# Optimization experiments

Measured on AMD Instinct MI355X. Metric: run time of the kernel, lower is better.

Reference implementation:

```python
import jax, jax.numpy as jnp
import numpy as np

C = 96        # dim
HEADS = 8     # FrameHistoryRouter heads (StateAlignBlock forces heads=1)
WS = 4        # window_size = 2*scale_patchsize
NFC = 1       # num_frames_tocache
TOPK = 5
LOCAL_N = 4


def conv(x, w, stride=1, pad=0, groups=1):
    return jax.lax.conv_general_dilated(
        x, w, (stride, stride), [(pad, pad), (pad, pad)],
        dimension_numbers=("NCHW", "OIHW", "NCHW"), feature_group_count=groups)


def l2norm(x, axis):
    n = jnp.linalg.norm(x, axis=axis, keepdims=True)
    return x / jnp.maximum(n, 1e-12)


def setup_inputs() -> dict:
    key = jax.random.key(0)
    ks = jax.random.split(key, 16)
    def rn(i, shp, s=0.02):
        return jax.random.normal(ks[i], shp, dtype=jnp.float32) * s
    return {
        "x": jax.random.normal(ks[0], (2, C, 256, 256), dtype=jnp.float32),
        "sab_qk_w": rn(1, (2 * C, C, 1, 1)),
        "sab_qk_dw": rn(2, (2 * C, 1, 3, 3)),
        "sab_v_w": rn(3, (C, C, 1, 1)),
        "sab_v_dw": rn(4, (C, 1, 3, 3)),
        "sab_k2_w": rn(5, (2 * C, C, 1, 1)),
        "sab_k2_dw": rn(6, (2 * C, 1, WS, WS)),
        "sab_q2_w": rn(7, (2 * C, C, 1, 1)),
        "sab_q2_dw": rn(8, (2 * C, 1, WS, WS)),
        "sab_proj_w": rn(9, (C, C, 1, 1)),
        "sab_temp": jnp.ones((1, 1, 1), jnp.float32),
        "fhr_qkv_w": rn(10, (3 * C, C, 1, 1)),
        "fhr_qkv_dw": rn(11, (3 * C, 1, 3, 3)),
        "fhr_proj_w": rn(12, (C, C, 1, 1)),
        "fhr_temp": jnp.ones((HEADS, 1, 1), jnp.float32),
    }


def _forward(x, sab_qk_w, sab_qk_dw, sab_v_w, sab_v_dw, sab_k2_w, sab_k2_dw,
             sab_q2_w, sab_q2_dw, sab_proj_w, sab_temp,
             fhr_qkv_w, fhr_qkv_dw, fhr_proj_w, fhr_temp):
    b, c, h, w = x.shape
    # ---------- StateAlignBlock (no cache: first frame) ----------
    qk = conv(conv(x, sab_qk_w), sab_qk_dw, pad=1, groups=2 * c)
    q, k = jnp.split(qk, 2, axis=1)
    v = conv(conv(x, sab_v_w), sab_v_dw, pad=1, groups=c)
    k = conv(conv(k, sab_k2_w), sab_k2_dw, stride=WS, pad=1, groups=2 * c)
    q = conv(conv(q, sab_q2_w), sab_q2_dw, stride=WS, pad=1, groups=2 * c)
    H, W = q.shape[2], q.shape[3]            # = h//WS, w//WS
    N = H * W
    # b (1 d) h w -> b 1 1 (h w) d   with d = 2c
    q = q.reshape(b, 2 * c, N).transpose(0, 2, 1)[:, None, None]
    k = k.reshape(b, 2 * c, N).transpose(0, 2, 1)[:, None, None]
    # v: b (1 d) (p1 h) (p2 w) -> b 1 1 (h w) (p1 p2 d), p1=p2=WS, d=c
    h2, w2 = h // WS, w // WS
    v = v.reshape(b, c, WS, h2, WS, w2).transpose(0, 3, 5, 2, 4, 1)
    v = v.reshape(b, 1, 1, h2 * w2, WS * WS * c)
    q = l2norm(q, -1)
    k = l2norm(k, -1)
    attn = jnp.einsum("bfgnd,bfgmd->bfgnm", q, k) * sab_temp  # [b,1,1,N,N]
    # zero_out_non_top_k (top-5 along last dim; threshold form, ties negligible)
    kth = jax.lax.top_k(attn, TOPK)[0][..., TOPK - 1:TOPK]
    topk_mask = (attn >= kth).astype(attn.dtype)
    # local attention mask: manhattan distance <= LOCAL_N on the HxW patch grid
    yy, xx = jnp.meshgrid(jnp.arange(H), jnp.arange(W), indexing="ij")
    coords = jnp.stack([yy.ravel(), xx.ravel()], axis=-1)          # [N,2]
    dist = jnp.abs(coords[:, None, :] - coords[None, :, :]).sum(-1)
    local = (dist <= LOCAL_N).astype(attn.dtype)                   # [N,N]
    attn = attn * topk_mask + attn * local                         # as in torch
    # clipped_softmax
    zero = attn == 0
    s = jax.nn.softmax(jnp.where(zero, -jnp.inf, attn), axis=-1)
    s = jnp.where(zero, 0.0, s)
    s = s / s.sum(-1, keepdims=True)
    out = jnp.einsum("bfgnm,bfgmd->bfgnd", s, v)  # [b,1,1,N, WS*WS*c]
    F = 1  # curr_num_frames (no cache)
    # b f 1 (h w) (p1 p2 d) -> (b f) d (p1 h) (p2 w)
    out = out.reshape(b * F, h2, w2, WS, WS, c).transpose(0, 5, 3, 1, 4, 2)
    out = out.reshape(b * F, c, h, w)
    out = conv(out, sab_proj_w)
    aligned = out.reshape(b, F, c, h, w)
    k_s = k[:, -NFC:]  # [b,1,1,N,2c]
    v_s = v[:, -NFC:]
    # ---------- FrameHistoryRouter on aligned current frame ----------
    x2 = aligned[:, -1]
    qkv = conv(conv(x2, fhr_qkv_w), fhr_qkv_dw, pad=1, groups=3 * c)
    q2, k2, v2 = jnp.split(qkv, 3, axis=1)
    hd = c // HEADS
    q2 = q2.reshape(b, HEADS, hd, h * w)
    k2 = k2.reshape(b, HEADS, hd, h * w)
    v2 = v2.reshape(b, HEADS, hd, h * w)
    q2 = l2norm(q2, -1)
    k2 = l2norm(k2, -1)
    a2 = jnp.einsum("bhcn,bhdn->bhcd", q2, k2) * fhr_temp  # [b,H,hd,hd]
    a2 = jax.nn.softmax(a2, axis=-1)
    o2 = jnp.einsum("bhcd,bhdn->bhcn", a2, v2).reshape(b, c, h, w)
    o2 = conv(o2, fhr_proj_w)
    keep = int(NFC * c / HEADS)  # = hd
    return o2, k_s, v_s, k2[:, :, -keep:, :], v2[:, :, -keep:, :]


def reference(x, sab_qk_w, sab_qk_dw, sab_v_w, sab_v_dw, sab_k2_w, sab_k2_dw,
              sab_q2_w, sab_q2_dw, sab_proj_w, sab_temp,
              fhr_qkv_w, fhr_qkv_dw, fhr_proj_w, fhr_temp):
    return _forward(x, sab_qk_w, sab_qk_dw, sab_v_w, sab_v_dw, sab_k2_w,
                    sab_k2_dw, sab_q2_w, sab_q2_dw, sab_proj_w, sab_temp,
                    fhr_qkv_w, fhr_qkv_dw, fhr_proj_w, fhr_temp)
```

## Files before the change

kernel.cpp:

```cpp
#include <hip/hip_runtime.h>
#include <hip/hip_bf16.h>
#include <math.h>

#define HW 65536L

typedef __attribute__((ext_vector_type(8))) short bf16x8;
typedef __attribute__((ext_vector_type(4))) float f32x4;

__device__ __forceinline__ int iabs_(int v) { return v < 0 ? -v : v; }

__global__ __launch_bounds__(256) void wsplit(
    const float* __restrict__ qk, const float* __restrict__ v,
    const float* __restrict__ q2, const float* __restrict__ k2,
    const float* __restrict__ pj, const float* __restrict__ fq,
    const float* __restrict__ fp, unsigned short* __restrict__ whl)
{
  const int e = blockIdx.x*256 + threadIdx.x;
  if (e >= 110592) return;
  const int row = e / 96, col = e - row*96;
  float f;
  if      (row <  192) f = qk[e];
  else if (row <  288) f = v [(row-192)*96+col];
  else if (row <  480) f = q2[(row-288)*96+col];
  else if (row <  672) f = k2[(row-480)*96+col];
  else if (row <  768) f = pj[(row-672)*96+col];
  else if (row < 1056) f = fq[(row-768)*96+col];
  else                 f = fp[(row-1056)*96+col];
  __hip_bfloat16 h = __float2bfloat16(f);
  float hf = __bfloat162float(h);
  __hip_bfloat16 l = __float2bfloat16(f - hf);
  whl[e]          = *(unsigned short*)&h;
  whl[110592 + e] = *(unsigned short*)&l;
}

#define BLDS 104
__global__ __launch_bounds__(256) void conv1x1_mfma(
    const float* __restrict__ in, long in_bstride,
    const unsigned short* __restrict__ whl, int wrow0,
    float* __restrict__ out, long out_bstride,
    float* __restrict__ out2, long out2_bstride, int msplit,
    int mtiles, int mode)
{
  __shared__ unsigned short bhs[128*BLDS];
  __shared__ unsigned short bls[128*BLDS];
  const int t = threadIdx.x;
  const int p0 = blockIdx.x * 128;
  const int b = blockIdx.y;
  if (mode == 0) {
    #pragma unroll
    for (int it = 0; it < 6; it++) {
      const int idx = it*256 + t;
      const int g8 = idx >> 7;
      const int pix = idx & 127;
      const float* src = in + (long)b*in_bstride + (long)(g8*8)*HW + p0 + pix;
      unsigned hh[8], ll[8];
      #pragma unroll
      for (int j = 0; j < 8; j++) {
        float f = src[(long)j*HW];
        unsigned u = __float_as_uint(f);
        hh[j] = u >> 16;
        float lof = f - __uint_as_float(u & 0xFFFF0000u);
        __hip_bfloat16 lb = __float2bfloat16(lof);
        ll[j] = *(unsigned short*)&lb;
      }
      uint4 hv, lv;
      hv.x = hh[0]|(hh[1]<<16); hv.y = hh[2]|(hh[3]<<16);
      hv.z = hh[4]|(hh[5]<<16); hv.w = hh[6]|(hh[7]<<16);
      lv.x = ll[0]|(ll[1]<<16); lv.y = ll[2]|(ll[3]<<16);
      lv.z = ll[4]|(ll[5]<<16); lv.w = ll[6]|(ll[7]<<16);
      *(uint4*)(bhs + pix*BLDS + g8*8) = hv;
      *(uint4*)(bls + pix*BLDS + g8*8) = lv;
    }
  } else {
    const int pp = t >> 1, half = (t & 1)*48;
    const int p = p0 + pp;
    const int py = p >> 8, px = p & 255;
    const float* src = in + (long)b*in_bstride
        + ((long)((py & 63)*64 + (px & 63))*16 + ((py >> 6)*4 + (px >> 6)))*96 + half;
    #pragma unroll
    for (int j4 = 0; j4 < 12; j4++) {
      float4 v4 = *(const float4*)&src[j4*4];
      float fv[4] = {v4.x, v4.y, v4.z, v4.w};
      unsigned hh[4], ll[4];
      #pragma unroll
      for (int u4 = 0; u4 < 4; u4++) {
        unsigned u = __float_as_uint(fv[u4]);
        hh[u4] = u >> 16;
        float lof = fv[u4] - __uint_as_float(u & 0xFFFF0000u);
        __hip_bfloat16 lb = __float2bfloat16(lof);
        ll[u4] = *(unsigned short*)&lb;
      }
      uint2 hv, lv;
      hv.x = hh[0] | (hh[1] << 16); hv.y = hh[2] | (hh[3] << 16);
      lv.x = ll[0] | (ll[1] << 16); lv.y = ll[2] | (ll[3] << 16);
      *(uint2*)(bhs + pp*BLDS + half + j4*4) = hv;
      *(uint2*)(bls + pp*BLDS + half + j4*4) = lv;
    }
  }
  __syncthreads();
  const int lane = t & 63, w = t >> 6;
  const int fr = lane & 15, fk = lane >> 4;
  bf16x8 Bh[2][3], Bl[2][3];
  #pragma unroll
  for (int nt = 0; nt < 2; nt++)
    #pragma unroll
    for (int kt = 0; kt < 3; kt++) {
      const int pix = w*32 + nt*16 + fr;
      Bh[nt][kt] = *(const bf16x8*)(bhs + pix*BLDS + kt*32 + fk*8);
      Bl[nt][kt] = *(const bf16x8*)(bls + pix*BLDS + kt*32 + fk*8);
    }
  for (int m = 0; m < mtiles; m++) {
    const long wbase = (long)(wrow0 + m*16 + fr)*96 + fk*8;
    bf16x8 Ah[3], Al[3];
    #pragma unroll
    for (int kt = 0; kt < 3; kt++) {
      Ah[kt] = *(const bf16x8*)(whl + wbase + kt*32);
      Al[kt] = *(const bf16x8*)(whl + 110592 + wbase + kt*32);
    }
    f32x4 acc[2] = {};
    #pragma unroll
    for (int nt = 0; nt < 2; nt++)
      #pragma unroll
      for (int kt = 0; kt < 3; kt++) {
        acc[nt] = __builtin_amdgcn_mfma_f32_16x16x32_bf16(Ah[kt], Bh[nt][kt], acc[nt], 0, 0, 0);
        acc[nt] = __builtin_amdgcn_mfma_f32_16x16x32_bf16(Ah[kt], Bl[nt][kt], acc[nt], 0, 0, 0);
        acc[nt] = __builtin_amdgcn_mfma_f32_16x16x32_bf16(Al[kt], Bh[nt][kt], acc[nt], 0, 0, 0);
      }
    const int mo = (m < msplit) ? m : (m - msplit);
    float* dst = ((m < msplit) ? out + (long)b*out_bstride
                               : out2 + (long)b*out2_bstride) + p0 + w*32;
    #pragma unroll
    for (int nt = 0; nt < 2; nt++)
      #pragma unroll
      for (int r = 0; r < 4; r++)
        dst[(long)(mo*16 + fk*4 + r)*HW + nt*16 + fr] = acc[nt][r];
  }
}

__global__ __launch_bounds__(256) void dw3x3v(
    const float* __restrict__ in, int inCH, const float* __restrict__ w,
    float* __restrict__ out, int outCH)
{
  const int t = threadIdx.x;
  const int p4 = blockIdx.x * 256 + t;
  const int ch = blockIdx.y, b = blockIdx.z;
  const int y = p4 >> 6, x0 = (p4 & 63) << 2;
  const float* ip = in + ((long)b*inCH + ch) * HW;
  const float* wp = w + ch*9;
  float a0 = 0.f, a1 = 0.f, a2 = 0.f, a3 = 0.f;
  #pragma unroll
  for (int dy = -1; dy <= 1; dy++) {
    const int yy = y + dy;
    if (yy < 0 || yy > 255) continue;
    const float* rp = ip + yy*256;
    const float4 c = *(const float4*)&rp[x0];
    const float left  = (x0 > 0)   ? rp[x0-1] : 0.f;
    const float right = (x0 < 252) ? rp[x0+4] : 0.f;
    const float w0 = wp[(dy+1)*3+0], w1 = wp[(dy+1)*3+1], w2 = wp[(dy+1)*3+2];
    a0 = fmaf(left, w0, a0); a0 = fmaf(c.x, w1, a0); a0 = fmaf(c.y, w2, a0);
    a1 = fmaf(c.x,  w0, a1); a1 = fmaf(c.y, w1, a1); a1 = fmaf(c.z, w2, a1);
    a2 = fmaf(c.y,  w0, a2); a2 = fmaf(c.z, w1, a2); a2 = fmaf(c.w, w2, a2);
    a3 = fmaf(c.z,  w0, a3); a3 = fmaf(c.w, w1, a3); a3 = fmaf(right, w2, a3);
  }
  float4 o; o.x = a0; o.y = a1; o.z = a2; o.w = a3;
  *(float4*)&out[((long)b*outCH + ch)*HW + y*256 + x0] = o;
}

__global__ __launch_bounds__(256) void dw3x3_vs(
    const float* __restrict__ in, const float* __restrict__ w,
    float* __restrict__ vs)
{
  __shared__ float tile[96*65];
  const int t = threadIdx.x;
  const int gb = blockIdx.x;
  const int b = blockIdx.y;
  const int y = gb >> 2, xb = gb & 3;
  #pragma unroll
  for (int i = 0; i < 6; i++) {
    const int idx = i*256 + t;
    const int ci = idx >> 4, q = idx & 15;
    const int x0 = xb*64 + q*4;
    const float* ip = in + ((long)b*96 + ci) * HW;
    const float* wp = w + ci*9;
    float a0 = 0.f, a1 = 0.f, a2 = 0.f, a3 = 0.f;
    #pragma unroll
    for (int dy = -1; dy <= 1; dy++) {
      const int yy = y + dy;
      if (yy < 0 || yy > 255) continue;
      const float* rp = ip + yy*256;
      const float4 c = *(const float4*)&rp[x0];
      const float left  = (x0 > 0)   ? rp[x0-1] : 0.f;
      const float right = (x0 < 252) ? rp[x0+4] : 0.f;
      const float w0 = wp[(dy+1)*3+0], w1 = wp[(dy+1)*3+1], w2 = wp[(dy+1)*3+2];
      a0 = fmaf(left, w0, a0); a0 = fmaf(c.x, w1, a0); a0 = fmaf(c.y, w2, a0);
      a1 = fmaf(c.x,  w0, a1); a1 = fmaf(c.y, w1, a1); a1 = fmaf(c.z, w2, a1);
      a2 = fmaf(c.y,  w0, a2); a2 = fmaf(c.z, w1, a2); a2 = fmaf(c.w, w2, a2);
      a3 = fmaf(c.z,  w0, a3); a3 = fmaf(c.w, w1, a3); a3 = fmaf(right, w2, a3);
    }
    const int xl = q*4;
    tile[ci*65 + xl    ] = a0;
    tile[ci*65 + xl + 1] = a1;
    tile[ci*65 + xl + 2] = a2;
    tile[ci*65 + xl + 3] = a3;
  }
  __syncthreads();
  const int blk = (y >> 6)*4 + xb;
  float* obase = vs + ((long)b*4096 + (long)(y & 63)*64) * 1536 + blk*96;
  #pragma unroll
  for (int i = 0; i < 24; i++) {
    const int idx = i*256 + t;
    const int nl = idx / 96, ci = idx % 96;
    obase[(long)nl*1536 + ci] = tile[ci*65 + nl];
  }
}

__global__ __launch_bounds__(256) void dw4x4s4v(
    const float* __restrict__ in, const float* __restrict__ w,
    float* __restrict__ out)
{
  const int t = threadIdx.x;
  const int p = blockIdx.x*256 + t;
  const int ch = blockIdx.y, b = blockIdx.z;
  const int oy = p >> 4, qx = p & 15;
  const int x0 = qx*16;
  const float* ip = in + (long)(b*192 + ch) * HW;
  const float* wp = w + ch*16;
  float a0 = 0.f, a1 = 0.f, a2 = 0.f, a3 = 0.f;
  #pragma unroll
  for (int ty = 0; ty < 4; ty++) {
    const int iy = 4*oy + ty - 1;
    if (iy < 0 || iy > 255) continue;
    const float* rp = ip + iy*256;
    float r[17];
    r[0] = (x0 > 0) ? rp[x0-1] : 0.f;
    #pragma unroll
    for (int k = 0; k < 4; k++) {
      float4 v4 = *(const float4*)&rp[x0 + k*4];
      r[1+k*4+0]=v4.x; r[1+k*4+1]=v4.y; r[1+k*4+2]=v4.z; r[1+k*4+3]=v4.w;
    }
    const float w0=wp[ty*4+0], w1=wp[ty*4+1], w2=wp[ty*4+2], w3=wp[ty*4+3];
    a0=fmaf(r[ 0],w0,a0); a0=fmaf(r[ 1],w1,a0); a0=fmaf(r[ 2],w2,a0); a0=fmaf(r[ 3],w3,a0);
    a1=fmaf(r[ 4],w0,a1); a1=fmaf(r[ 5],w1,a1); a1=fmaf(r[ 6],w2,a1); a1=fmaf(r[ 7],w3,a1);
    a2=fmaf(r[ 8],w0,a2); a2=fmaf(r[ 9],w1,a2); a2=fmaf(r[10],w2,a2); a2=fmaf(r[11],w3,a2);
    a3=fmaf(r[12],w0,a3); a3=fmaf(r[13],w1,a3); a3=fmaf(r[14],w2,a3); a3=fmaf(r[15],w3,a3);
  }
  float4 o; o.x=a0; o.y=a1; o.z=a2; o.w=a3;
  *(float4*)&out[(long)(b*192 + ch)*4096 + oy*64 + qx*4] = o;
}

__global__ __launch_bounds__(256) void l2n192(
    const float* __restrict__ inA, float* __restrict__ outA,
    const float* __restrict__ inB, float* __restrict__ outB)
{
  const int t = threadIdx.x;
  const int wid = t >> 6, lane = t & 63;
  const int gw2 = blockIdx.x * 4 + wid;
  const int sel = gw2 >> 13;
  const int gw = gw2 & 8191;
  const int b = gw >> 12, n = gw & 4095;
  const float* ip = (sel ? inB : inA) + (long)b * 786432;
  float v0 = ip[(long)(lane      ) * 4096 + n];
  float v1 = ip[(long)(lane +  64) * 4096 + n];
  float v2 = ip[(long)(lane + 128) * 4096 + n];
  float ss = v0*v0 + v1*v1 + v2*v2;
  #pragma unroll
  for (int s = 1; s < 64; s <<= 1) ss += __shfl_xor(ss, s, 64);
  float nrm = fmaxf(sqrtf(ss), 1e-12f);
  float* op = (sel ? outB : outA) + ((long)b*4096 + n) * 192;
  op[lane      ] = v0 / nrm;
  op[lane +  64] = v1 / nrm;
  op[lane + 128] = v2 / nrm;
}

__global__ __launch_bounds__(256) void bf16split(
    const float* __restrict__ in, unsigned short* __restrict__ outp)
{
  const int i = blockIdx.x * 256 + threadIdx.x;
  const int n = i / 192, k = i % 192;
  float f = in[i];
  __hip_bfloat16 h = __float2bfloat16(f);
  float hf = __bfloat162float(h);
  __hip_bfloat16 l = __float2bfloat16(f - hf);
  outp[(long)n*384 + k]       = *(unsigned short*)&h;
  outp[(long)n*384 + 192 + k] = *(unsigned short*)&l;
}

#define LDSROW 40
__global__ __launch_bounds__(256) void attn_qk_mfma(
    const unsigned short* __restrict__ Qsp, const unsigned short* __restrict__ Ksp,
    float* __restrict__ attn, const float* __restrict__ tp)
{
  __shared__ unsigned short qs[256*LDSROW];
  __shared__ unsigned short ks[256*LDSROW];
  const int t = threadIdx.x;
  const int lane = t & 63, w = t >> 6;
  const int n0 = blockIdx.x * 128;
  const int m0 = blockIdx.y * 128;
  const int wr = (w >> 1) * 64, wc = (w & 1) * 64;
  f32x4 acc[4][4] = {};
  const int srow = t & 127;
  const int shl  = t >> 7;
  const unsigned short* qsrc = Qsp + (long)(n0 + srow) * 384 + shl * 192;
  const unsigned short* ksrc = Ksp + (long)(m0 + srow) * 384 + shl * 192;
  unsigned short* qdst = qs + (shl*128 + srow) * LDSROW;
  unsigned short* kdst = ks + (shl*128 + srow) * LDSROW;
  const int fr = lane & 15;
  const int fk = lane >> 4;
  for (int s = 0; s < 6; s++) {
    __syncthreads();
    #pragma unroll
    for (int j = 0; j < 4; j++) {
      *(bf16x8*)(qdst + j*8) = *(const bf16x8*)(qsrc + s*32 + j*8);
      *(bf16x8*)(kdst + j*8) = *(const bf16x8*)(ksrc + s*32 + j*8);
    }
    __syncthreads();
    bf16x8 ah[4], al[4], bh[4], bl[4];
    #pragma unroll
    for (int i = 0; i < 4; i++) {
      ah[i] = *(const bf16x8*)(qs + (      wr + i*16 + fr) * LDSROW + fk*8);
      al[i] = *(const bf16x8*)(qs + (128 + wr + i*16 + fr) * LDSROW + fk*8);
      bh[i] = *(const bf16x8*)(ks + (      wc + i*16 + fr) * LDSROW + fk*8);
      bl[i] = *(const bf16x8*)(ks + (128 + wc + i*16 + fr) * LDSROW + fk*8);
    }
    #pragma unroll
    for (int i = 0; i < 4; i++)
      #pragma unroll
      for (int j = 0; j < 4; j++) {
        acc[i][j] = __builtin_amdgcn_mfma_f32_16x16x32_bf16(ah[i], bh[j], acc[i][j], 0, 0, 0);
        acc[i][j] = __builtin_amdgcn_mfma_f32_16x16x32_bf16(ah[i], bl[j], acc[i][j], 0, 0, 0);
        acc[i][j] = __builtin_amdgcn_mfma_f32_16x16x32_bf16(al[i], bh[j], acc[i][j], 0, 0, 0);
      }
  }
  const float temp = tp[0];
  #pragma unroll
  for (int i = 0; i < 4; i++)
    #pragma unroll
    for (int j = 0; j < 4; j++)
      #pragma unroll
      for (int r = 0; r < 4; r++) {
        const int nn = n0 + wr + i*16 + (lane >> 4)*4 + r;
        const int mm = m0 + wc + j*16 + (lane & 15);
        attn[(long)nn*4096 + mm] = acc[i][j][r] * temp;
      }
}

#define CAP 128
__global__ __launch_bounds__(256) void attn_out_k(
    const float* __restrict__ attn, const float* __restrict__ vs,
    float* __restrict__ outr)
{
  __shared__ float row[4096];
  __shared__ float top5[256*5];
  __shared__ int   lm[CAP];
  __shared__ float lw[CAP];
  __shared__ float ses[CAP];
  __shared__ float redf[8];
  __shared__ int   wsum[4];
  const int t = threadIdx.x;
  const int n = blockIdx.x;
  const float* ar = attn + (long)n * 4096;
  #pragma unroll
  for (int k = 0; k < 16; k++) row[k*256 + t] = ar[k*256 + t];
  __syncthreads();
  float t0=-INFINITY,t1=-INFINITY,t2=-INFINITY,t3=-INFINITY,t4=-INFINITY;
  #pragma unroll
  for (int k = 0; k < 16; k++) {
    float v = row[k*256 + t];
    if (v > t4) {
      if (v > t0)      { t4=t3; t3=t2; t2=t1; t1=t0; t0=v; }
      else if (v > t1) { t4=t3; t3=t2; t2=t1; t1=v; }
      else if (v > t2) { t4=t3; t3=t2; t2=v; }
      else if (v > t3) { t4=t3; t3=v; }
      else             { t4=v; }
    }
  }
  top5[t*5+0]=t0; top5[t*5+1]=t1; top5[t*5+2]=t2; top5[t*5+3]=t3; top5[t*5+4]=t4;
  __syncthreads();
  for (int s = 128; s >= 1; s >>= 1) {
    if (t < s) {
      float* A = &top5[t*5];
      const float* B = &top5[(t+s)*5];
      float m[5]; int i = 0, j = 0;
      #pragma unroll
      for (int k = 0; k < 5; k++) {
        float av = A[i], bv = B[j];
        if (av >= bv) { m[k] = av; i++; } else { m[k] = bv; j++; }
      }
      #pragma unroll
      for (int k = 0; k < 5; k++) A[k] = m[k];
    }
    __syncthreads();
  }
  const float kth = top5[4];
  const int y = n >> 6, x = n & 63;
  int myc = 0;
  float wmax = -INFINITY;
  #pragma unroll
  for (int k = 0; k < 16; k++) {
    int m = k*256 + t;
    float a = row[m];
    int c = ((a >= kth) ? 1 : 0) +
            (((iabs_(y - (m >> 6)) + iabs_(x - (m & 63))) <= 4) ? 1 : 0);
    float wv = a * (float)c;
    if (wv != 0.0f) { myc++; wmax = fmaxf(wmax, wv); }
  }
  int inc = myc;
  #pragma unroll
  for (int s = 1; s < 64; s <<= 1) {
    int v = __shfl_up(inc, s, 64);
    if ((t & 63) >= s) inc += v;
  }
  if ((t & 63) == 63) wsum[t >> 6] = inc;
  __syncthreads();
  int pre = 0;
  #pragma unroll
  for (int wj = 0; wj < 4; wj++) pre += (wj < (t >> 6)) ? wsum[wj] : 0;
  const int base = pre + inc - myc;
  const int cnt = wsum[0] + wsum[1] + wsum[2] + wsum[3];
  {
    int idx = base;
    #pragma unroll
    for (int k = 0; k < 16; k++) {
      int m = k*256 + t;
      float a = row[m];
      int c = ((a >= kth) ? 1 : 0) +
              (((iabs_(y - (m >> 6)) + iabs_(x - (m & 63))) <= 4) ? 1 : 0);
      float wv = a * (float)c;
      if (wv != 0.0f && idx < CAP) { lm[idx] = m; lw[idx] = wv; idx++; }
    }
  }
  #pragma unroll
  for (int s = 1; s < 64; s <<= 1) wmax = fmaxf(wmax, __shfl_xor(wmax, s, 64));
  if ((t & 63) == 0) redf[t >> 6] = wmax;
  __syncthreads();
  const float gmax = fmaxf(fmaxf(redf[0], redf[1]), fmaxf(redf[2], redf[3]));
  __syncthreads();
  if (t < cnt && t < CAP) ses[t] = expf(lw[t] - gmax);
  __syncthreads();
  float ps = (t < cnt && t < CAP) ? ses[t] : 0.f;
  #pragma unroll
  for (int s = 1; s < 64; s <<= 1) ps += __shfl_xor(ps, s, 64);
  if ((t & 63) == 0) redf[4 + (t >> 6)] = ps;
  __syncthreads();
  const float S = redf[4] + redf[5] + redf[6] + redf[7];
  const float invS = 1.0f / S;
  float a0=0,a1=0,a2=0,a3=0,a4=0,a5=0;
  const int ecnt = (cnt < CAP) ? cnt : CAP;
  for (int e = 0; e < ecnt; e++) {
    float se = ses[e] * invS;
    const float* vr = vs + (long)lm[e] * 1536;
    a0 = fmaf(se, vr[        t], a0);
    a1 = fmaf(se, vr[ 256 + t], a1);
    a2 = fmaf(se, vr[ 512 + t], a2);
    a3 = fmaf(se, vr[ 768 + t], a3);
    a4 = fmaf(se, vr[1024 + t], a4);
    a5 = fmaf(se, vr[1280 + t], a5);
  }
  float* orow = outr + (long)n * 1536;
  orow[        t] = a0;
  orow[ 256 + t] = a1;
  orow[ 512 + t] = a2;
  orow[ 768 + t] = a3;
  orow[1024 + t] = a4;
  orow[1280 + t] = a5;
}

__global__ __launch_bounds__(1024) void l2n_sp(
    const float* __restrict__ in, float* __restrict__ out)
{
  const int ch = blockIdx.x, b = blockIdx.y, t = threadIdx.x;
  const float* ip = in + ((long)b*96 + ch) * HW;
  float ss = 0.f;
  for (int i = t; i < 65536; i += 1024) { float v = ip[i]; ss = fmaf(v, v, ss); }
  __shared__ float red[16];
  #pragma unroll
  for (int s = 1; s < 64; s <<= 1) ss += __shfl_xor(ss, s, 64);
  if ((t & 63) == 0) red[t >> 6] = ss;
  __syncthreads();
  if (t == 0) {
    float s2 = 0.f;
    for (int i = 0; i < 16; i++) s2 += red[i];
    red[0] = fmaxf(sqrtf(s2), 1e-12f);
  }
  __syncthreads();
  const float nrm = red[0];
  float* op = out + ((long)b*96 + ch) * HW;
  for (int i = t; i < 65536; i += 1024) op[i] = ip[i] / nrm;
}

#define A2_NCH 16
__global__ __launch_bounds__(256) void a2_part(
    const float* __restrict__ q2n, const float* __restrict__ k2n,
    float* __restrict__ part, float* __restrict__ qqpart)
{
  __shared__ float sh[24*260];
  const int t = threadIdx.x;
  const int ch = blockIdx.x, h = blockIdx.y, b = blockIdx.z;
  const long base = ((long)b*96 + h*12) * HW + ch*4096;
  const int c = t / 12, d = t - (t/12)*12;
  float acc = 0.f;
  float qq = 0.f;
  for (int sub = 0; sub < 16; sub++) {
    __syncthreads();
    #pragma unroll
    for (int j = 0; j < 6; j++) {
      const int v = j*256 + t;
      const int row = v >> 6;
      const int col4 = v & 63;
      const float* src = (row < 12)
        ? q2n + base + (long)row*HW + sub*256 + col4*4
        : k2n + base + (long)(row-12)*HW + sub*256 + col4*4;
      *(float4*)&sh[row*260 + col4*4] = *(const float4*)src;
    }
    __syncthreads();
    if (t < 144) {
      const float* qr = &sh[c*260];
      const float* kr = &sh[(12+d)*260];
      #pragma unroll
      for (int i4 = 0; i4 < 64; i4++) {
        float4 qv = *(const float4*)&qr[i4*4];
        float4 kv = *(const float4*)&kr[i4*4];
        acc = fmaf(qv.x, kv.x, acc);
        acc = fmaf(qv.y, kv.y, acc);
        acc = fmaf(qv.z, kv.z, acc);
        acc = fmaf(qv.w, kv.w, acc);
      }
    } else if (t < 156) {
      const float* qr = &sh[(t-144)*260];
      #pragma unroll
      for (int i4 = 0; i4 < 64; i4++) {
        float4 qv = *(const float4*)&qr[i4*4];
        qq = fmaf(qv.x, qv.x, qq);
        qq = fmaf(qv.y, qv.y, qq);
        qq = fmaf(qv.z, qv.z, qq);
        qq = fmaf(qv.w, qv.w, qq);
      }
    }
  }
  if (t < 144)
    part[(((long)b*8 + h)*A2_NCH + ch)*144 + t] = acc;
  else if (t < 156)
    qqpart[(((long)b*8 + h)*A2_NCH + ch)*12 + (t-144)] = qq;
}

__global__ __launch_bounds__(256) void a2_fin(
    const float* __restrict__ part, const float* __restrict__ qqpart,
    const float* __restrict__ temp, float* __restrict__ a2s)
{
  __shared__ float m[144];
  __shared__ float qn[12];
  const int t = threadIdx.x;
  const int h = blockIdx.x, b = blockIdx.y;
  if (t < 144) {
    float s = 0.f;
    const float* pp = part + (((long)b*8 + h)*A2_NCH)*144 + t;
    #pragma unroll
    for (int ch = 0; ch < A2_NCH; ch++) s += pp[ch*144];
    m[t] = s;
  } else if (t < 156) {
    float s = 0.f;
    const float* pp = qqpart + (((long)b*8 + h)*A2_NCH)*12 + (t-144);
    #pragma unroll
    for (int ch = 0; ch < A2_NCH; ch++) s += pp[ch*12];
    qn[t-144] = fmaxf(sqrtf(s), 1e-12f);
  }
  __syncthreads();
  if (t < 12) {
    const float tv = temp[h];
    const float scale = tv / qn[t];
    float mx = -INFINITY;
    float a[12];
    #pragma unroll
    for (int d = 0; d < 12; d++) { a[d] = m[t*12+d] * scale; mx = fmaxf(mx, a[d]); }
    float e[12], sum = 0.f;
    #pragma unroll
    for (int d = 0; d < 12; d++) { e[d] = expf(a[d]-mx); sum += e[d]; }
    float inv = 1.0f/sum;
    float* op = a2s + (((long)b*8 + h)*12 + t)*12;
    #pragma unroll
    for (int d = 0; d < 12; d++) op[d] = e[d]*inv;
  }
}

__global__ __launch_bounds__(256) void o2pre_kern(
    const float* __restrict__ a2s, const float* __restrict__ v2,
    float* __restrict__ o2p)
{
  const int t = threadIdx.x;
  const int n = blockIdx.x * 256 + t;
  const int bh = blockIdx.y, b = bh >> 3, h = bh & 7;
  const float* a = a2s + (long)bh * 144;
  const float* vb = v2 + ((long)b*96 + h*12) * HW;
  float vv[12];
  #pragma unroll
  for (int d = 0; d < 12; d++) vv[d] = vb[(long)d*HW + n];
  float* ob = o2p + ((long)b*96 + h*12) * HW;
  #pragma unroll
  for (int c = 0; c < 12; c++) {
    float s = 0.f;
    #pragma unroll
    for (int d = 0; d < 12; d++) s = fmaf(a[c*12 + d], vv[d], s);
    ob[(long)c*HW + n] = s;
  }
}

extern "C" void kernel_launch(void* const* d_in, const int* in_sizes, int n_in,
                              void* d_out, int out_size, void* d_ws, size_t ws_size,
                              hipStream_t stream) {
  const float* x        = (const float*)d_in[0];
  const float* qk_w     = (const float*)d_in[1];
  const float* qk_dw    = (const float*)d_in[2];
  const float* v_w      = (const float*)d_in[3];
  const float* v_dw     = (const float*)d_in[4];
  const float* k2_w     = (const float*)d_in[5];
  const float* k2_dw    = (const float*)d_in[6];
  const float* q2_w     = (const float*)d_in[7];
  const float* q2_dw    = (const float*)d_in[8];
  const float* proj_w   = (const float*)d_in[9];
  const float* sab_temp = (const float*)d_in[10];
  const float* fqkv_w   = (const float*)d_in[11];
  const float* fqkv_dw  = (const float*)d_in[12];
  const float* fproj_w  = (const float*)d_in[13];
  const float* fhr_temp = (const float*)d_in[14];
  float* out = (float*)d_out;
  float* ws  = (float*)d_ws;

  float* O2  = out;
  float* KS  = out + 12582912;
  float* VS  = out + 14155776;
  float* K2N = out + 26738688;
  float* V2  = out + 39321600;

  float* A0   = ws;
  float* A1   = ws + 25165824;
  float* QD   = ws + 50331648;
  float* KD   = ws + 51904512;
  float* QN   = ws + 53477376;
  float* A2S  = ws + 55050240;
  float* PART = ws + 55052544;
  unsigned short* QSP = (unsigned short*)(A0 + 16777216);
  unsigned short* KSP = (unsigned short*)(A0 + 16777216 + 786432);
  unsigned short* WHL = (unsigned short*)QN;
  float* ALN = ws;
  float* PRE = ws + 12582912;
  float* OB  = ws + 12582912;
  float* QQP = QD;

  dim3 b256(256), b1024(1024);

  wsplit<<<dim3(432), b256, 0, stream>>>(qk_w, v_w, q2_w, k2_w, proj_w, fqkv_w, fproj_w, WHL);
  conv1x1_mfma<<<dim3(512,2), b256, 0, stream>>>(
      x, 96L*HW, WHL, 0, A0, 192L*HW, A1, 96L*HW, 12, 18, 0);
  dw3x3_vs<<<dim3(1024,2), b256, 0, stream>>>(A1, v_dw, VS);
  dw3x3v<<<dim3(64,192,2), b256, 0, stream>>>(A0, 192, qk_dw, A1, 192);
  conv1x1_mfma<<<dim3(512,2), b256, 0, stream>>>(
      A1, 192L*HW, WHL, 288, A0, 192L*HW, A0, 192L*HW, 12, 12, 0);
  dw4x4s4v<<<dim3(4,192,2), b256, 0, stream>>>(A0, q2_dw, QD);
  conv1x1_mfma<<<dim3(512,2), b256, 0, stream>>>(
      A1 + 96L*HW, 192L*HW, WHL, 480, A0, 192L*HW, A0, 192L*HW, 12, 12, 0);
  dw4x4s4v<<<dim3(4,192,2), b256, 0, stream>>>(A0, k2_dw, KD);
  l2n192<<<dim3(4096), b256, 0, stream>>>(QD, QN, KD, KS);
  for (int b = 0; b < 2; b++) {
    bf16split<<<dim3(3072), b256, 0, stream>>>(QN + (long)b*786432, QSP);
    bf16split<<<dim3(3072), b256, 0, stream>>>(KS + (long)b*786432, KSP);
    attn_qk_mfma<<<dim3(32,32), b256, 0, stream>>>(QSP, KSP, A0, sab_temp);
    attn_out_k<<<dim3(4096), b256, 0, stream>>>(
        A0, VS + (long)b*6291456, A1 + (long)b*6291456);
  }
  wsplit<<<dim3(432), b256, 0, stream>>>(qk_w, v_w, q2_w, k2_w, proj_w, fqkv_w, fproj_w, WHL);
  conv1x1_mfma<<<dim3(512,2), b256, 0, stream>>>(
      A1, 6291456L, WHL, 672, ALN, 96L*HW, ALN, 96L*HW, 6, 6, 1);
  conv1x1_mfma<<<dim3(512,2), b256, 0, stream>>>(
      ALN, 96L*HW, WHL, 768, PRE, 288L*HW, PRE, 288L*HW, 18, 18, 0);
  dw3x3v<<<dim3(64,96,2), b256, 0, stream>>>(PRE,            288, fqkv_dw,        ALN, 96);
  dw3x3v<<<dim3(64,96,2), b256, 0, stream>>>(PRE +  96L*HW, 288, fqkv_dw +  864, K2N, 96);
  dw3x3v<<<dim3(64,96,2), b256, 0, stream>>>(PRE + 192L*HW, 288, fqkv_dw + 1728, V2,  96);
  l2n_sp<<<dim3(96,2), b1024, 0, stream>>>(K2N, K2N);
  a2_part<<<dim3(A2_NCH,8,2), b256, 0, stream>>>(ALN, K2N, PART, QQP);
  a2_fin<<<dim3(8,2), b256, 0, stream>>>(PART, QQP, fhr_temp, A2S);
  o2pre_kern<<<dim3(256,16), b256, 0, stream>>>(A2S, V2, OB);
  conv1x1_mfma<<<dim3(512,2), b256, 0, stream>>>(
      OB, 96L*HW, WHL, 1056, O2, 96L*HW, O2, 96L*HW, 6, 6, 0);
}
```

Before: 871.5 us.

## Fold 1x1 convolution weight products to remove intermediate full-resolution passes

Precomputes the product of the FrameHistoryRouter qkv weights and the StateAlign projection weights, so one 1x1 conv on the attention output produces q/k/v directly. The separate projection pass and its full-resolution intermediate go away. It also folds the per-head softmax attention matrix into the final projection weights with a per-batch weight kernel, which removes o2pre_kern and its full read/write of V2. The cost is extra small weight-composition kernels and a change in rounding order, since the composed weights are split into bf16 hi/lo pairs.

```diff
diff --git a/kernel.cpp b/kernel.cpp
--- a/kernel.cpp
+++ b/kernel.cpp
@@ -9,37 +9,69 @@
 
 __device__ __forceinline__ int iabs_(int v) { return v < 0 ? -v : v; }
 
+__device__ __forceinline__ void rtn_split(float f, unsigned short* h, unsigned short* l) {
+  __hip_bfloat16 hb = __float2bfloat16(f);
+  float hf = __bfloat162float(hb);
+  __hip_bfloat16 lb = __float2bfloat16(f - hf);
+  *h = *(unsigned short*)&hb;
+  *l = *(unsigned short*)&lb;
+}
+
 __global__ __launch_bounds__(256) void wsplit(
     const float* __restrict__ qk, const float* __restrict__ v,
     const float* __restrict__ q2, const float* __restrict__ k2,
-    const float* __restrict__ pj, const float* __restrict__ fq,
-    const float* __restrict__ fp, unsigned short* __restrict__ whl)
+    unsigned short* __restrict__ whl)
 {
   const int e = blockIdx.x*256 + threadIdx.x;
-  if (e >= 110592) return;
+  if (e >= 64512) return;
   const int row = e / 96, col = e - row*96;
   float f;
   if      (row <  192) f = qk[e];
   else if (row <  288) f = v [(row-192)*96+col];
   else if (row <  480) f = q2[(row-288)*96+col];
-  else if (row <  672) f = k2[(row-480)*96+col];
-  else if (row <  768) f = pj[(row-672)*96+col];
-  else if (row < 1056) f = fq[(row-768)*96+col];
-  else                 f = fp[(row-1056)*96+col];
-  __hip_bfloat16 h = __float2bfloat16(f);
-  float hf = __bfloat162float(h);
-  __hip_bfloat16 l = __float2bfloat16(f - hf);
-  whl[e]          = *(unsigned short*)&h;
-  whl[110592 + e] = *(unsigned short*)&l;
+  else                 f = k2[(row-480)*96+col];
+  rtn_split(f, &whl[e], &whl[110592 + e]);
+}
+
+__global__ __launch_bounds__(256) void wcomp1(
+    const float* __restrict__ fq, const float* __restrict__ pj,
+    unsigned short* __restrict__ whl)
+{
+  const int e = blockIdx.x*256 + threadIdx.x;
+  if (e >= 27648) return;
+  const int row = e / 96, col = e - row*96;
+  float s = 0.f;
+  #pragma unroll 8
+  for (int c = 0; c < 96; c++) s = fmaf(fq[row*96 + c], pj[c*96 + col], s);
+  rtn_split(s, &whl[(768+row)*96 + col], &whl[110592 + (768+row)*96 + col]);
+}
+
+__global__ __launch_bounds__(256) void wcomp2(
+    const float* __restrict__ fp, const float* __restrict__ a2s,
+    unsigned short* __restrict__ w2)
+{
+  const int e = blockIdx.x*256 + threadIdx.x;
+  const int b = blockIdx.y;
+  if (e >= 9216) return;
+  const int co = e / 96, dg = e - co*96;
+  const int h = dg / 12, d = dg - h*12;
+  const float* ab = a2s + (((long)b*8 + h)*12)*12 + d;
+  const float* fpb = fp + co*96 + h*12;
+  float s = 0.f;
+  #pragma unroll
+  for (int c = 0; c < 12; c++) s = fmaf(fpb[c], ab[c*12], s);
+  rtn_split(s, &w2[(long)b*9216 + e], &w2[18432 + (long)b*9216 + e]);
 }
 
 #define BLDS 104
 __global__ __launch_bounds__(256) void conv1x1_mfma(
     const float* __restrict__ in, long in_bstride,
-    const unsigned short* __restrict__ whl, int wrow0,
+    const unsigned short* __restrict__ whl_hi, const unsigned short* __restrict__ whl_lo,
+    long wbstride, int wrow0,
     float* __restrict__ out, long out_bstride,
-    float* __restrict__ out2, long out2_bstride, int msplit,
-    int mtiles, int mode)
+    float* __restrict__ out2, long out2_bstride,
+    float* __restrict__ out3, long out3_bstride,
+    int ms1, int ms2, int mtiles, int mode)
 {
   __shared__ unsigned short bhs[128*BLDS];
   __shared__ unsigned short bls[128*BLDS];
@@ -109,13 +141,14 @@
       Bh[nt][kt] = *(const bf16x8*)(bhs + pix*BLDS + kt*32 + fk*8);
       Bl[nt][kt] = *(const bf16x8*)(bls + pix*BLDS + kt*32 + fk*8);
     }
+  const long wb = (long)b*wbstride;
   for (int m = 0; m < mtiles; m++) {
-    const long wbase = (long)(wrow0 + m*16 + fr)*96 + fk*8;
+    const long wbase = wb + (long)(wrow0 + m*16 + fr)*96 + fk*8;
     bf16x8 Ah[3], Al[3];
     #pragma unroll
     for (int kt = 0; kt < 3; kt++) {
-      Ah[kt] = *(const bf16x8*)(whl + wbase + kt*32);
-      Al[kt] = *(const bf16x8*)(whl + 110592 + wbase + kt*32);
+      Ah[kt] = *(const bf16x8*)(whl_hi + wbase + kt*32);
+      Al[kt] = *(const bf16x8*)(whl_lo + wbase + kt*32);
     }
     f32x4 acc[2] = {};
     #pragma unroll
@@ -126,9 +159,11 @@
         acc[nt] = __builtin_amdgcn_mfma_f32_16x16x32_bf16(Ah[kt], Bl[nt][kt], acc[nt], 0, 0, 0);
         acc[nt] = __builtin_amdgcn_mfma_f32_16x16x32_bf16(Al[kt], Bh[nt][kt], acc[nt], 0, 0, 0);
       }
-    const int mo = (m < msplit) ? m : (m - msplit);
-    float* dst = ((m < msplit) ? out + (long)b*out_bstride
-                               : out2 + (long)b*out2_bstride) + p0 + w*32;
+    int mo; float* dst;
+    if (m < ms1)      { mo = m;       dst = out  + (long)b*out_bstride; }
+    else if (m < ms2) { mo = m - ms1; dst = out2 + (long)b*out2_bstride; }
+    else              { mo = m - ms2; dst = out3 + (long)b*out3_bstride; }
+    dst += p0 + w*32;
     #pragma unroll
     for (int nt = 0; nt < 2; nt++)
       #pragma unroll
@@ -278,11 +313,10 @@
   const int i = blockIdx.x * 256 + threadIdx.x;
   const int n = i / 192, k = i % 192;
   float f = in[i];
-  __hip_bfloat16 h = __float2bfloat16(f);
-  float hf = __bfloat162float(h);
-  __hip_bfloat16 l = __float2bfloat16(f - hf);
-  outp[(long)n*384 + k]       = *(unsigned short*)&h;
-  outp[(long)n*384 + 192 + k] = *(unsigned short*)&l;
+  unsigned short h, l;
+  rtn_split(f, &h, &l);
+  outp[(long)n*384 + k]       = h;
+  outp[(long)n*384 + 192 + k] = l;
 }
 
 #define LDSROW 40
@@ -579,28 +613,6 @@
     float* op = a2s + (((long)b*8 + h)*12 + t)*12;
     #pragma unroll
     for (int d = 0; d < 12; d++) op[d] = e[d]*inv;
-  }
-}
-
-__global__ __launch_bounds__(256) void o2pre_kern(
-    const float* __restrict__ a2s, const float* __restrict__ v2,
-    float* __restrict__ o2p)
-{
-  const int t = threadIdx.x;
-  const int n = blockIdx.x * 256 + t;
-  const int bh = blockIdx.y, b = bh >> 3, h = bh & 7;
-  const float* a = a2s + (long)bh * 144;
-  const float* vb = v2 + ((long)b*96 + h*12) * HW;
-  float vv[12];
-  #pragma unroll
-  for (int d = 0; d < 12; d++) vv[d] = vb[(long)d*HW + n];
-  float* ob = o2p + ((long)b*96 + h*12) * HW;
-  #pragma unroll
-  for (int c = 0; c < 12; c++) {
-    float s = 0.f;
-    #pragma unroll
-    for (int d = 0; d < 12; d++) s = fmaf(a[c*12 + d], vv[d], s);
-    ob[(long)c*HW + n] = s;
   }
 }
 
@@ -641,23 +653,28 @@
   unsigned short* QSP = (unsigned short*)(A0 + 16777216);
   unsigned short* KSP = (unsigned short*)(A0 + 16777216 + 786432);
   unsigned short* WHL = (unsigned short*)QN;
-  float* ALN = ws;
-  float* PRE = ws + 12582912;
-  float* OB  = ws + 12582912;
+  float* P1  = ws;
+  float* P2  = ws + 12582912;
+  float* P3  = ws + 37748736;
+  float* ALNQ = P2;
   float* QQP = QD;
+  unsigned short* W2HL = (unsigned short*)PART;
 
   dim3 b256(256), b1024(1024);
 
-  wsplit<<<dim3(432), b256, 0, stream>>>(qk_w, v_w, q2_w, k2_w, proj_w, fqkv_w, fproj_w, WHL);
+  wsplit<<<dim3(252), b256, 0, stream>>>(qk_w, v_w, q2_w, k2_w, WHL);
   conv1x1_mfma<<<dim3(512,2), b256, 0, stream>>>(
-      x, 96L*HW, WHL, 0, A0, 192L*HW, A1, 96L*HW, 12, 18, 0);
+      x, 96L*HW, WHL, WHL+110592, 0, 0,
+      A0, 192L*HW, A1, 96L*HW, A1, 96L*HW, 12, 18, 18, 0);
   dw3x3_vs<<<dim3(1024,2), b256, 0, stream>>>(A1, v_dw, VS);
   dw3x3v<<<dim3(64,192,2), b256, 0, stream>>>(A0, 192, qk_dw, A1, 192);
   conv1x1_mfma<<<dim3(512,2), b256, 0, stream>>>(
-      A1, 192L*HW, WHL, 288, A0, 192L*HW, A0, 192L*HW, 12, 12, 0);
+      A1, 192L*HW, WHL, WHL+110592, 0, 288,
+      A0, 192L*HW, A0, 192L*HW, A0, 192L*HW, 12, 12, 12, 0);
   dw4x4s4v<<<dim3(4,192,2), b256, 0, stream>>>(A0, q2_dw, QD);
   conv1x1_mfma<<<dim3(512,2), b256, 0, stream>>>(
-      A1 + 96L*HW, 192L*HW, WHL, 480, A0, 192L*HW, A0, 192L*HW, 12, 12, 0);
+      A1 + 96L*HW, 192L*HW, WHL, WHL+110592, 0, 480,
+      A0, 192L*HW, A0, 192L*HW, A0, 192L*HW, 12, 12, 12, 0);
   dw4x4s4v<<<dim3(4,192,2), b256, 0, stream>>>(A0, k2_dw, KD);
   l2n192<<<dim3(4096), b256, 0, stream>>>(QD, QN, KD, KS);
   for (int b = 0; b < 2; b++) {
@@ -667,18 +684,18 @@
     attn_out_k<<<dim3(4096), b256, 0, stream>>>(
         A0, VS + (long)b*6291456, A1 + (long)b*6291456);
   }
-  wsplit<<<dim3(432), b256, 0, stream>>>(qk_w, v_w, q2_w, k2_w, proj_w, fqkv_w, fproj_w, WHL);
+  wcomp1<<<dim3(108), b256, 0, stream>>>(fqkv_w, proj_w, WHL);
   conv1x1_mfma<<<dim3(512,2), b256, 0, stream>>>(
-      A1, 6291456L, WHL, 672, ALN, 96L*HW, ALN, 96L*HW, 6, 6, 1);
+      A1, 6291456L, WHL, WHL+110592, 0, 768,
+      P1, 96L*HW, P2, 96L*HW, P3, 96L*HW, 6, 12, 18, 1);
+  dw3x3v<<<dim3(64,96,2), b256, 0, stream>>>(P2, 96, fqkv_dw +  864, K2N, 96);
+  dw3x3v<<<dim3(64,96,2), b256, 0, stream>>>(P3, 96, fqkv_dw + 1728, V2,  96);
+  dw3x3v<<<dim3(64,96,2), b256, 0, stream>>>(P1, 96, fqkv_dw,        ALNQ, 96);
+  l2n_sp<<<dim3(96,2), b1024, 0, stream>>>(K2N, K2N);
+  a2_part<<<dim3(A2_NCH,8,2), b256, 0, stream>>>(ALNQ, K2N, PART, QQP);
+  a2_fin<<<dim3(8,2), b256, 0, stream>>>(PART, QQP, fhr_temp, A2S);
+  wcomp2<<<dim3(36,2), b256, 0, stream>>>(fproj_w, A2S, W2HL);
   conv1x1_mfma<<<dim3(512,2), b256, 0, stream>>>(
-      ALN, 96L*HW, WHL, 768, PRE, 288L*HW, PRE, 288L*HW, 18, 18, 0);
-  dw3x3v<<<dim3(64,96,2), b256, 0, stream>>>(PRE,            288, fqkv_dw,        ALN, 96);
-  dw3x3v<<<dim3(64,96,2), b256, 0, stream>>>(PRE +  96L*HW, 288, fqkv_dw +  864, K2N, 96);
-  dw3x3v<<<dim3(64,96,2), b256, 0, stream>>>(PRE + 192L*HW, 288, fqkv_dw + 1728, V2,  96);
-  l2n_sp<<<dim3(96,2), b1024, 0, stream>>>(K2N, K2N);
-  a2_part<<<dim3(A2_NCH,8,2), b256, 0, stream>>>(ALN, K2N, PART, QQP);
-  a2_fin<<<dim3(8,2), b256, 0, stream>>>(PART, QQP, fhr_temp, A2S);
-  o2pre_kern<<<dim3(256,16), b256, 0, stream>>>(A2S, V2, OB);
-  conv1x1_mfma<<<dim3(512,2), b256, 0, stream>>>(
-      OB, 96L*HW, WHL, 1056, O2, 96L*HW, O2, 96L*HW, 6, 6, 0);
-}
+      V2, 96L*HW, W2HL, W2HL+18432, 9216, 0,
+      O2, 96L*HW, O2, 96L*HW, O2, 96L*HW, 6, 6, 6, 0);
+}
```

Measured after the change: 831.3 us. -4.6%, faster.
